# Performance work log

Hardware: AMD Instinct MI355X
Metric: run time of the kernel (lower is better)

## Reference

```python
import jax, jax.numpy as jnp
import numpy as np

N_HEAD, D_MODEL, D_HEAD = 16, 1024, 64
LN_EPS = 1e-5


def setup_inputs() -> dict:
    key = jax.random.key(0)
    ks = jax.random.split(key, 12)
    S, B = 1024, 8
    nd = N_HEAD * D_HEAD
    sc = 0.02
    return {
        "hidden_states": jax.random.normal(ks[0], (S, B, D_MODEL), jnp.float32),
        "rel_pos_emb": jax.random.normal(ks[1], (S, D_MODEL), jnp.float32),
        "encoder_hidden_states": jax.random.normal(ks[2], (S, B, D_MODEL), jnp.float32),
        "W_q": jax.random.normal(ks[3], (D_MODEL, nd), jnp.float32) * sc,
        "W_kv": jax.random.normal(ks[4], (D_MODEL, 2 * nd), jnp.float32) * sc,
        "W_r": jax.random.normal(ks[5], (D_MODEL, nd), jnp.float32) * sc,
        "W_o": jax.random.normal(ks[6], (nd, D_MODEL), jnp.float32) * sc,
        "r_w_bias": jax.random.normal(ks[7], (N_HEAD, D_HEAD), jnp.float32) * sc,
        "r_r_bias": jax.random.normal(ks[8], (N_HEAD, D_HEAD), jnp.float32) * sc,
        "ln_gamma": jnp.ones((D_MODEL,), jnp.float32),
        "ln_beta": jnp.zeros((D_MODEL,), jnp.float32),
    }


def _rel_shift(x):
    # x: (qlen, rlen, bsz, n_head) -- Transformer-XL relative shift trick
    q, r, b, n = x.shape
    zero_pad = jnp.zeros((q, 1, b, n), x.dtype)
    x_padded = jnp.concatenate([zero_pad, x], axis=1).reshape(r + 1, q, b, n)
    return x_padded[1:].reshape(q, r, b, n)


def _layer_norm(x, gamma, beta):
    mu = jnp.mean(x, axis=-1, keepdims=True)
    var = jnp.mean(jnp.square(x - mu), axis=-1, keepdims=True)
    return (x - mu) * jax.lax.rsqrt(var + LN_EPS) * gamma + beta


def reference(hidden_states, rel_pos_emb, encoder_hidden_states,
              W_q, W_kv, W_r, W_o, r_w_bias, r_r_bias, ln_gamma, ln_beta):
    qlen, bsz, _ = hidden_states.shape
    rlen = rel_pos_emb.shape[0]
    # post-lnorm path (pre_lnorm=False), no mems, no mask, eval (dropout off)
    mem_heads = encoder_hidden_states @ W_kv            # (klen, b, 2*n*d)
    w_head_q = hidden_states @ W_q                      # (qlen, b, n*d)
    r_head_k = rel_pos_emb @ W_r                        # (rlen, n*d)
    w_head_k, w_head_v = jnp.split(mem_heads, 2, axis=-1)
    klen = w_head_k.shape[0]

    w_head_q = w_head_q.reshape(qlen, bsz, N_HEAD, D_HEAD)
    w_head_k = w_head_k.reshape(klen, bsz, N_HEAD, D_HEAD)
    w_head_v = w_head_v.reshape(klen, bsz, N_HEAD, D_HEAD)
    r_head_k = r_head_k.reshape(rlen, N_HEAD, D_HEAD)

    scale = 1.0 / (D_HEAD ** 0.5)
    AC = jnp.einsum('ibnd,jbnd->ijbn', w_head_q + r_w_bias, w_head_k)
    BD = jnp.einsum('ibnd,jnd->ijbn', w_head_q + r_r_bias, r_head_k)
    BD = _rel_shift(BD)
    attn_score = (AC + BD) * scale                      # (q, k, b, n)

    attn_prob = jax.nn.softmax(attn_score, axis=1)
    attn_vec = jnp.einsum('ijbn,jbnd->ibnd', attn_prob, w_head_v)
    attn_vec = attn_vec.reshape(qlen, bsz, N_HEAD * D_HEAD)
    attn_out = attn_vec @ W_o
    return _layer_norm(hidden_states + attn_out, ln_gamma, ln_beta)
```

## Files before the change

kernel.cpp:

```cpp
#include <hip/hip_runtime.h>
#include <stdint.h>

constexpr int SEQ = 1024;
constexpr int BSZ = 8;
constexpr int NHEAD = 16;
constexpr int DHEAD = 64;
constexpr int DMODEL = 1024;

using u16 = unsigned short;
using bf16x8 = __attribute__((ext_vector_type(8))) short;
using f32x4 = __attribute__((ext_vector_type(4))) float;

__device__ __forceinline__ float bf2f(u16 u) {
  union { unsigned int i; float f; } c; c.i = ((unsigned int)u) << 16; return c.f;
}
__device__ __forceinline__ unsigned cvtpk(float a, float b) {
  unsigned r; asm("v_cvt_pk_bf16_f32 %0, %1, %2" : "=v"(r) : "v"(a), "v"(b)); return r;
}
__device__ __forceinline__ float exp2v(float x) {
  float r; asm("v_exp_f32 %0, %1" : "=v"(r) : "v"(x)); return r;
}
__device__ __forceinline__ void gload16(const void* g, void* l) {
  __builtin_amdgcn_global_load_lds((const __attribute__((address_space(1))) void*)g,
                                   (__attribute__((address_space(3))) void*)l, 16, 0, 0);
}
__device__ __forceinline__ bf16x8 cvt8(const float* src) {
  f32x4 a = *(const f32x4*)src;
  f32x4 b = *(const f32x4*)(src + 4);
  union { unsigned u[4]; bf16x8 v; } o;
  o.u[0] = cvtpk(a[0], a[1]); o.u[1] = cvtpk(a[2], a[3]);
  o.u[2] = cvtpk(b[0], b[1]); o.u[3] = cvtpk(b[2], b[3]);
  return o.v;
}
__device__ __forceinline__ bf16x8 rd8(const u16* base, int row, int col) {
  return *(const bf16x8*)((const char*)base + (((row * 64 + col) * 2) ^ ((row & 7) << 4)));
}
__device__ __forceinline__ bf16x8 rd8_128(const u16* base, int row, int col) {
  return *(const bf16x8*)((const char*)base + (((row * 128 + col) * 2) ^ ((row & 7) << 4)));
}
__device__ __forceinline__ void wr128(u16* base, int row, int col, u16 v) {
  *(u16*)((char*)base + (((row * 128 + col) * 2) ^ ((row & 7) << 4))) = v;
}

__device__ __forceinline__ void gemm_body_a32(
    const float* __restrict__ A, const u16* __restrict__ BT, u16* __restrict__ C,
    int ldc, int bx, int by, u16* As, u16* Bs) {
  const int t = threadIdx.x;
  const int lane = t & 63;
  const int w = t >> 6, wr = w >> 1, wc = w & 1;
  const int l15 = lane & 15, l4 = lane >> 4;
  const int row0 = by * 128, col0 = bx * 128;
  f32x4 acc[4][4] = {};
  for (int k0 = 0; k0 < 1024; k0 += 64) {
#pragma unroll
    for (int q = 0; q < 4; q++) {
      int u = q * 256 + t;
      int r = u >> 3, c8 = u & 7;
      int sc8 = c8 ^ (r & 7);
      int ub = (q * 256 + (t & ~63)) * 8;
      gload16(BT + (size_t)(col0 + r) * 1024 + k0 + sc8 * 8, Bs + ub);
      const float* src = A + (size_t)(row0 + r) * 1024 + k0 + sc8 * 8;
      *(bf16x8*)(As + (size_t)u * 8) = cvt8(src);
    }
    __syncthreads();
#pragma unroll
    for (int kk = 0; kk < 2; kk++) {
      bf16x8 av[4], bv[4];
#pragma unroll
      for (int f = 0; f < 4; f++) {
        int kb = kk * 32 + l4 * 8;
        av[f] = rd8(As, wr * 64 + f * 16 + l15, kb);
        bv[f] = rd8(Bs, wc * 64 + f * 16 + l15, kb);
      }
#pragma unroll
      for (int fr = 0; fr < 4; fr++)
#pragma unroll
        for (int fc = 0; fc < 4; fc++)
          acc[fr][fc] = __builtin_amdgcn_mfma_f32_16x16x32_bf16(av[fr], bv[fc], acc[fr][fc], 0, 0, 0);
    }
    __syncthreads();
  }
#pragma unroll
  for (int fr = 0; fr < 4; fr++)
#pragma unroll
    for (int fc = 0; fc < 4; fc++) {
      int col = col0 + wc * 64 + fc * 16 + l15;
      int rw0 = row0 + wr * 64 + fr * 16 + l4 * 4;
      unsigned p01 = cvtpk(acc[fr][fc][0], acc[fr][fc][1]);
      unsigned p23 = cvtpk(acc[fr][fc][2], acc[fr][fc][3]);
      C[(size_t)(rw0 + 0) * ldc + col] = (u16)p01;
      C[(size_t)(rw0 + 1) * ldc + col] = (u16)(p01 >> 16);
      C[(size_t)(rw0 + 2) * ldc + col] = (u16)p23;
      C[(size_t)(rw0 + 3) * ldc + col] = (u16)(p23 >> 16);
    }
}

__global__ __launch_bounds__(256, 2) void gemm3(
    const float* __restrict__ hidden, const float* __restrict__ enc,
    const float* __restrict__ relpos,
    const u16* __restrict__ WQT, const u16* __restrict__ WKVT, const u16* __restrict__ WRT,
    u16* __restrict__ Qb, u16* __restrict__ KVb, u16* __restrict__ Rh) {
  __shared__ __align__(16) u16 As[128 * 64];
  __shared__ __align__(16) u16 Bs[128 * 64];
  const int bid = blockIdx.x;
  const float* A; const u16* BT; u16* C; int ldc, bx, by;
  if (bid < 512)       { A = hidden; BT = WQT;  C = Qb;  ldc = 1024; bx = bid & 7;  by = bid >> 3; }
  else if (bid < 1536) { int r = bid - 512;  A = enc;    BT = WKVT; C = KVb; ldc = 2048; bx = r & 15; by = r >> 4; }
  else                 { int r = bid - 1536; A = relpos; BT = WRT;  C = Rh;  ldc = 1024; bx = r & 7;  by = r >> 3; }
  gemm_body_a32(A, BT, C, ldc, bx, by, As, Bs);
}

__global__ __launch_bounds__(256, 2) void gemm_o(
    const u16* __restrict__ Ap, const u16* __restrict__ BT, float* __restrict__ Cp) {
  __shared__ __align__(16) u16 As[128 * 64];
  __shared__ __align__(16) u16 Bs[128 * 64];
  const int t = threadIdx.x;
  const int lane = t & 63;
  const int w = t >> 6, wr = w >> 1, wc = w & 1;
  const int l15 = lane & 15, l4 = lane >> 4;
  const int row0 = blockIdx.y * 128, col0 = blockIdx.x * 128;
  f32x4 acc[4][4] = {};
  for (int k0 = 0; k0 < 1024; k0 += 64) {
#pragma unroll
    for (int q = 0; q < 4; q++) {
      int u = q * 256 + t;
      int r = u >> 3, c8 = u & 7;
      int sc8 = c8 ^ (r & 7);
      int ub = (q * 256 + (t & ~63)) * 8;
      gload16(BT + (size_t)(col0 + r) * 1024 + k0 + sc8 * 8, Bs + ub);
      gload16(Ap + (size_t)(row0 + r) * 1024 + k0 + sc8 * 8, As + ub);
    }
    __syncthreads();
#pragma unroll
    for (int kk = 0; kk < 2; kk++) {
      bf16x8 av[4], bv[4];
#pragma unroll
      for (int f = 0; f < 4; f++) {
        int kb = kk * 32 + l4 * 8;
        av[f] = rd8(As, wr * 64 + f * 16 + l15, kb);
        bv[f] = rd8(Bs, wc * 64 + f * 16 + l15, kb);
      }
#pragma unroll
      for (int fr = 0; fr < 4; fr++)
#pragma unroll
        for (int fc = 0; fc < 4; fc++)
          acc[fr][fc] = __builtin_amdgcn_mfma_f32_16x16x32_bf16(av[fr], bv[fc], acc[fr][fc], 0, 0, 0);
    }
    __syncthreads();
  }
#pragma unroll
  for (int fr = 0; fr < 4; fr++)
#pragma unroll
    for (int fc = 0; fc < 4; fc++) {
      int col = col0 + wc * 64 + fc * 16 + l15;
      int rw0 = row0 + wr * 64 + fr * 16 + l4 * 4;
#pragma unroll
      for (int r = 0; r < 4; r++)
        Cp[(size_t)(rw0 + r) * 1024 + col] = acc[fr][fc][r];
    }
}

__global__ void corr_kernel(const u16* __restrict__ Rh, const float* __restrict__ rwb,
                            const float* __restrict__ rrb, float* __restrict__ corrR) {
  const int m0 = blockIdx.x * 64, n = blockIdx.y;
  const int t = threadIdx.x, r = t >> 2, q = t & 3;
  float p = 0.f;
#pragma unroll
  for (int e = 0; e < 16; e++) {
    int d = q * 16 + e;
    p += (rrb[n * DHEAD + d] - rwb[n * DHEAD + d]) * bf2f(Rh[(size_t)(m0 + r) * DMODEL + n * DHEAD + d]);
  }
  p += __shfl_xor(p, 1, 4);
  p += __shfl_xor(p, 2, 4);
  if (q == 0) corrR[n * SEQ + m0 + r] = p;
}

__global__ __launch_bounds__(256, 3) void flash_fused(
    const u16* __restrict__ Qb, const u16* __restrict__ KVb,
    const u16* __restrict__ VT, const u16* __restrict__ Rh,
    const float* __restrict__ rwb, const float* __restrict__ corrR,
    u16* __restrict__ AV) {
  __shared__ __align__(16) char smem[49408];
  u16* Qs = (u16*)smem;
  u16* Ks = (u16*)(smem + 8320);
  u16* Vs = (u16*)(smem + 16512);
  u16* Rs = (u16*)(smem + 24704);
  u16* Df = (u16*)(smem + 32896);
  const int t = threadIdx.x;
  const int lane = t & 63;
  const int w = t >> 6;
  const int l15 = lane & 15, l4 = lane >> 4;
  const int bid = blockIdx.x;
  const int sw = (bid & 7) * 256 + (bid >> 3);
  const int i0 = (sw & 15) * 64;
  const int z = sw >> 4, b = z >> 4, n = z & 15;
  const float KSC = 0.18033688f;

#pragma unroll
  for (int p = 0; p < 3; p++) {
    int u = p * 256 + t;
    if (u < 520) {
      int r = u >> 3, c8 = u & 7;
      int sc8 = c8 ^ (r & 7);
      int rq = i0 + r; if (rq > SEQ - 1) rq = SEQ - 1;
      bf16x8 qv = *(const bf16x8*)(Qb + ((size_t)rq * BSZ + b) * DMODEL + n * DHEAD + sc8 * 8);
      f32x4 b0 = *(const f32x4*)(rwb + n * DHEAD + sc8 * 8);
      f32x4 b1 = *(const f32x4*)(rwb + n * DHEAD + sc8 * 8 + 4);
      union { unsigned u4[4]; bf16x8 v; } o;
      o.u4[0] = cvtpk(bf2f((u16)qv[0]) + b0[0], bf2f((u16)qv[1]) + b0[1]);
      o.u4[1] = cvtpk(bf2f((u16)qv[2]) + b0[2], bf2f((u16)qv[3]) + b0[3]);
      o.u4[2] = cvtpk(bf2f((u16)qv[4]) + b1[0], bf2f((u16)qv[5]) + b1[1]);
      o.u4[3] = cvtpk(bf2f((u16)qv[6]) + b1[2], bf2f((u16)qv[7]) + b1[3]);
      *(bf16x8*)(Qs + (size_t)u * 8) = o.v;
    }
  }
  const int baseP = (SEQ - 64) - i0;
  const float* corrn = corrR + n * SEQ;
#pragma unroll
  for (int q = 0; q < 2; q++) {
    int u = q * 256 + t;
    int r = u >> 3, c8 = u & 7;
    int sc8 = c8 ^ (r & 7);
    int ub = (q * 256 + (t & ~63)) * 8;
    gload16(Rh + (size_t)(baseP + r) * DMODEL + n * DHEAD + sc8 * 8, Rs + ub);
  }
  float cP[4];
#pragma unroll
  for (int fc = 0; fc < 4; fc++) cP[fc] = corrn[baseP + fc * 16 + l15];
  __syncthreads();
  {
    f32x4 dp[4] = {};
#pragma unroll
    for (int kk = 0; kk < 2; kk++) {
      int kb = kk * 32 + l4 * 8;
      bf16x8 aQ = rd8(Qs, w * 16 + l15, kb);
#pragma unroll
      for (int fc = 0; fc < 4; fc++)
        dp[fc] = __builtin_amdgcn_mfma_f32_16x16x32_bf16(aQ, rd8(Rs, fc * 16 + l15, kb), dp[fc], 0, 0, 0);
    }
#pragma unroll
    for (int r = 0; r < 4; r++) {
      int row = w * 16 + l4 * 4 + r;
      unsigned d01 = cvtpk(dp[0][r] + cP[0], dp[1][r] + cP[1]);
      unsigned d23 = cvtpk(dp[2][r] + cP[2], dp[3][r] + cP[3]);
      wr128(Df, row, 0 * 16 + l15, (u16)d01);
      wr128(Df, row, 1 * 16 + l15, (u16)(d01 >> 16));
      wr128(Df, row, 2 * 16 + l15, (u16)d23);
      wr128(Df, row, 3 * 16 + l15, (u16)(d23 >> 16));
    }
  }
  f32x4 O[4] = {};
  float M[4], Lp[4];
#pragma unroll
  for (int r = 0; r < 4; r++) { M[r] = -1e30f; Lp[r] = 0.f; }
  float spec = 0.f;

  for (int jj = 0; jj < 16; jj++) {
    const int j0 = jj * 64;
    const int dlt = j0 - i0;
    const int base2 = (dlt < 0) ? dlt + SEQ : dlt;
    const int qo2 = (dlt >= 0) ? 1 : 0;
    const int off = (jj & 1) << 6;
    __syncthreads();
#pragma unroll
    for (int q = 0; q < 2; q++) {
      int u = q * 256 + t;
      int r = u >> 3, c8 = u & 7;
      int sc8 = c8 ^ (r & 7);
      int ub = (q * 256 + (t & ~63)) * 8;
      gload16(KVb + ((size_t)(j0 + r) * BSZ + b) * (2 * DMODEL) + n * DHEAD + sc8 * 8, Ks + ub);
      gload16(VT + ((size_t)(b * NHEAD + n) * DHEAD + r) * SEQ + j0 + sc8 * 8, Vs + ub);
      gload16(Rh + (size_t)(base2 + r) * DMODEL + n * DHEAD + sc8 * 8, Rs + ub);
    }
    float cr[4];
#pragma unroll
    for (int fc = 0; fc < 4; fc++) cr[fc] = corrn[base2 + fc * 16 + l15];
    __syncthreads();
    f32x4 sacc[4] = {}, dnew[4] = {};
    __builtin_amdgcn_s_setprio(1);
#pragma unroll
    for (int kk = 0; kk < 2; kk++) {
      int kb = kk * 32 + l4 * 8;
      int qr0 = w * 16 + l15;
      bf16x8 aQ = rd8(Qs, qr0, kb);
      bf16x8 aD = rd8(Qs, qr0 + qo2, kb);
#pragma unroll
      for (int fc = 0; fc < 4; fc++) {
        int br = fc * 16 + l15;
        sacc[fc] = __builtin_amdgcn_mfma_f32_16x16x32_bf16(aQ, rd8(Ks, br, kb), sacc[fc], 0, 0, 0);
        dnew[fc] = __builtin_amdgcn_mfma_f32_16x16x32_bf16(aD, rd8(Rs, br, kb), dnew[fc], 0, 0, 0);
      }
    }
    __builtin_amdgcn_s_setprio(0);
    const int offn = off ^ 64;
#pragma unroll
    for (int r = 0; r < 4; r++) {
      int row = w * 16 + l4 * 4 + r;
      unsigned d01 = cvtpk(dnew[0][r] + cr[0], dnew[1][r] + cr[1]);
      unsigned d23 = cvtpk(dnew[2][r] + cr[2], dnew[3][r] + cr[3]);
      wr128(Df, row, offn + 0 * 16 + l15, (u16)d01);
      wr128(Df, row, offn + 1 * 16 + l15, (u16)(d01 >> 16));
      wr128(Df, row, offn + 2 * 16 + l15, (u16)d23);
      wr128(Df, row, offn + 3 * 16 + l15, (u16)(d23 >> 16));
    }
    float specnext = 0.f;
    if (w == 3)
      specnext = bf2f(*(const u16*)((const char*)Df + ((63 * 256) | ((((off + 63) * 2) ^ 0x70)))));
    const float fix = (dlt == 64) ? 0.f : spec;
#pragma unroll
    for (int r = 0; r < 4; r++) {
      const int lrow = w * 16 + l4 * 4 + r;
      const int rbase = lrow * 256;
      const int swz = (lrow & 7) << 4;
      float v2[4];
      if (dlt < 0) {
        const int K = off + 63 - lrow;
#pragma unroll
        for (int fc = 0; fc < 4; fc++) {
          int col = (fc * 16 + l15 + K) & 127;
          float bd = bf2f(*(const u16*)((const char*)Df + (rbase | ((col * 2) ^ swz))));
          v2[fc] = (sacc[fc][r] + bd) * KSC;
        }
      } else if (dlt == 0) {
#pragma unroll
        for (int fc = 0; fc < 4; fc++) {
          int dj = fc * 16 + l15 - lrow;
          int ul = (dj <= 0) ? dj + 63 : dj + 62;
          int col = (off + ul) & 127;
          float bd = bf2f(*(const u16*)((const char*)Df + (rbase | ((col * 2) ^ swz))));
          if (dj == 1) bd = 0.f;
          v2[fc] = (sacc[fc][r] + bd) * KSC;
        }
      } else {
        const int K = 62 - lrow;
#pragma unroll
        for (int fc = 0; fc < 4; fc++) {
          int ul = fc * 16 + l15 + K;
          int col = (off + ((ul < 0) ? 0 : ul)) & 127;
          float bd = bf2f(*(const u16*)((const char*)Df + (rbase | ((col * 2) ^ swz))));
          if (ul < 0) bd = fix;
          v2[fc] = (sacc[fc][r] + bd) * KSC;
        }
      }
      float tm = fmaxf(fmaxf(v2[0], v2[1]), fmaxf(v2[2], v2[3]));
      unsigned long long bal = __ballot(tm > M[r] + 11.5f);
      if ((bal >> (l4 * 16)) & 0xFFFFull) {
        for (int mk = 1; mk < 16; mk <<= 1) tm = fmaxf(tm, __shfl_xor(tm, mk, 16));
        float alpha = exp2v(M[r] - tm);
        Lp[r] *= alpha;
#pragma unroll
        for (int fd = 0; fd < 4; fd++) O[fd][r] *= alpha;
        M[r] = tm;
      }
      float e0 = exp2v(v2[0] - M[r]), e1 = exp2v(v2[1] - M[r]);
      float e2 = exp2v(v2[2] - M[r]), e3 = exp2v(v2[3] - M[r]);
      Lp[r] += (e0 + e1) + (e2 + e3);
      unsigned p01 = cvtpk(e0, e1), p23 = cvtpk(e2, e3);
      wr128(Df, lrow, off + 0 * 16 + l15, (u16)p01);
      wr128(Df, lrow, off + 1 * 16 + l15, (u16)(p01 >> 16));
      wr128(Df, lrow, off + 2 * 16 + l15, (u16)p23);
      wr128(Df, lrow, off + 3 * 16 + l15, (u16)(p23 >> 16));
    }
    spec = specnext;
    __builtin_amdgcn_s_setprio(1);
#pragma unroll
    for (int kk = 0; kk < 2; kk++) {
      int kb = kk * 32 + l4 * 8;
      bf16x8 a = rd8_128(Df, w * 16 + l15, off + kb);
#pragma unroll
      for (int fd = 0; fd < 4; fd++)
        O[fd] = __builtin_amdgcn_mfma_f32_16x16x32_bf16(a, rd8(Vs, fd * 16 + l15, kb), O[fd], 0, 0, 0);
    }
    __builtin_amdgcn_s_setprio(0);
  }
  float Lf[4];
#pragma unroll
  for (int r = 0; r < 4; r++) {
    float Lt = Lp[r];
    for (int mk = 1; mk < 16; mk <<= 1) Lt += __shfl_xor(Lt, mk, 16);
    Lf[r] = 1.f / Lt;
  }
#pragma unroll
  for (int fd = 0; fd < 4; fd++) {
    int d = fd * 16 + l15;
    int iq0 = i0 + w * 16 + l4 * 4;
    unsigned p01 = cvtpk(O[fd][0] * Lf[0], O[fd][1] * Lf[1]);
    unsigned p23 = cvtpk(O[fd][2] * Lf[2], O[fd][3] * Lf[3]);
    AV[((size_t)(iq0 + 0) * BSZ + b) * DMODEL + n * DHEAD + d] = (u16)p01;
    AV[((size_t)(iq0 + 1) * BSZ + b) * DMODEL + n * DHEAD + d] = (u16)(p01 >> 16);
    AV[((size_t)(iq0 + 2) * BSZ + b) * DMODEL + n * DHEAD + d] = (u16)p23;
    AV[((size_t)(iq0 + 3) * BSZ + b) * DMODEL + n * DHEAD + d] = (u16)(p23 >> 16);
  }
}

__global__ void wtrans4(const float* __restrict__ W_q, const float* __restrict__ W_kv,
                        const float* __restrict__ W_r, const float* __restrict__ W_o,
                        u16* __restrict__ WQT, u16* __restrict__ WKVT,
                        u16* __restrict__ WRT, u16* __restrict__ WOT) {
  __shared__ unsigned int lds[64][65];
  const int bid = blockIdx.x;
  const float* in; u16* out; int C, cx, cy;
  if (bid < 256)      { in = W_q;  out = WQT;  C = 1024; cx = bid & 15;        cy = bid >> 4; }
  else if (bid < 768) { in = W_kv; out = WKVT; C = 2048; cx = (bid - 256) & 31; cy = (bid - 256) >> 5; }
  else if (bid < 1024){ in = W_r;  out = WRT;  C = 1024; cx = (bid - 768) & 15; cy = (bid - 768) >> 4; }
  else                { in = W_o;  out = WOT;  C = 1024; cx = (bid - 1024) & 15; cy = (bid - 1024) >> 4; }
  const int R = 1024;
  const int t = threadIdx.x;
  const int c0 = cx * 64, r0 = cy * 64;
#pragma unroll
  for (int p = 0; p < 2; p++) {
    int u = p * 256 + t;
    int r = u >> 3, c8 = u & 7;
    const float* src = in + (size_t)(r0 + r) * C + c0 + c8 * 8;
    f32x4 v0 = *(const f32x4*)src;
    f32x4 v1 = *(const f32x4*)(src + 4);
    unsigned q0 = cvtpk(v0[0], v0[1]), q1 = cvtpk(v0[2], v0[3]);
    unsigned q2 = cvtpk(v1[0], v1[1]), q3 = cvtpk(v1[2], v1[3]);
    lds[r][c8 * 8 + 0] = (u16)q0; lds[r][c8 * 8 + 1] = (u16)(q0 >> 16);
    lds[r][c8 * 8 + 2] = (u16)q1; lds[r][c8 * 8 + 3] = (u16)(q1 >> 16);
    lds[r][c8 * 8 + 4] = (u16)q2; lds[r][c8 * 8 + 5] = (u16)(q2 >> 16);
    lds[r][c8 * 8 + 6] = (u16)q3; lds[r][c8 * 8 + 7] = (u16)(q3 >> 16);
  }
  __syncthreads();
#pragma unroll
  for (int p = 0; p < 2; p++) {
    int u = p * 256 + t;
    int r = u >> 3, c8 = u & 7;
    bf16x8 v;
#pragma unroll
    for (int e = 0; e < 8; e++) v[e] = (short)lds[c8 * 8 + e][r];
    *(bf16x8*)(out + (size_t)(c0 + r) * R + r0 + c8 * 8) = v;
  }
}

__global__ void vtrans(const u16* __restrict__ KVb, u16* __restrict__ VT) {
  __shared__ unsigned int lds[64][65];
  const int t = threadIdx.x;
  const int s0 = blockIdx.x * 64, n = blockIdx.y, b = blockIdx.z;
#pragma unroll
  for (int p = 0; p < 2; p++) {
    int u = p * 256 + t;
    int r = u >> 3, c8 = u & 7;
    const u16* src = KVb + ((size_t)(s0 + r) * BSZ + b) * (2 * DMODEL) + DMODEL + n * DHEAD + c8 * 8;
    bf16x8 v = *(const bf16x8*)src;
#pragma unroll
    for (int e = 0; e < 8; e++) lds[r][c8 * 8 + e] = (u16)v[e];
  }
  __syncthreads();
#pragma unroll
  for (int p = 0; p < 2; p++) {
    int u = p * 256 + t;
    int r = u >> 3, c8 = u & 7;
    bf16x8 v;
#pragma unroll
    for (int e = 0; e < 8; e++) v[e] = (short)lds[c8 * 8 + e][r];
    *(bf16x8*)(VT + ((size_t)(b * NHEAD + n) * DHEAD + r) * SEQ + s0 + c8 * 8) = v;
  }
}

__global__ void ln_kernel(const float* __restrict__ hidden,
                          const float* __restrict__ gamma, const float* __restrict__ beta,
                          float* __restrict__ out) {
  __shared__ float wsum[4];
  __shared__ float wvar[4];
  const int row = blockIdx.x;
  const int t = threadIdx.x;
  f32x4 hv = *(const f32x4*)(hidden + (size_t)row * DMODEL + t * 4);
  f32x4 ov = *(const f32x4*)(out + (size_t)row * DMODEL + t * 4);
  float xs[4], sum = 0.f;
#pragma unroll
  for (int e = 0; e < 4; e++) { xs[e] = hv[e] + ov[e]; sum += xs[e]; }
  for (int mk = 1; mk < 64; mk <<= 1) sum += __shfl_xor(sum, mk, 64);
  if ((t & 63) == 0) wsum[t >> 6] = sum;
  __syncthreads();
  float mu = (wsum[0] + wsum[1] + wsum[2] + wsum[3]) * (1.f / DMODEL);
  float var = 0.f;
#pragma unroll
  for (int e = 0; e < 4; e++) { float d = xs[e] - mu; var += d * d; }
  for (int mk = 1; mk < 64; mk <<= 1) var += __shfl_xor(var, mk, 64);
  if ((t & 63) == 0) wvar[t >> 6] = var;
  __syncthreads();
  float rstd = rsqrtf((wvar[0] + wvar[1] + wvar[2] + wvar[3]) * (1.f / DMODEL) + 1e-5f);
  f32x4 res;
#pragma unroll
  for (int e = 0; e < 4; e++) {
    int c = t * 4 + e;
    res[e] = (xs[e] - mu) * rstd * gamma[c] + beta[c];
  }
  *(f32x4*)(out + (size_t)row * DMODEL + t * 4) = res;
}

extern "C" void kernel_launch(void* const* d_in, const int* in_sizes, int n_in,
                              void* d_out, int out_size, void* d_ws, size_t ws_size,
                              hipStream_t stream) {
  const float* hidden = (const float*)d_in[0];
  const float* relpos = (const float*)d_in[1];
  const float* enc    = (const float*)d_in[2];
  const float* W_q    = (const float*)d_in[3];
  const float* W_kv   = (const float*)d_in[4];
  const float* W_r    = (const float*)d_in[5];
  const float* W_o    = (const float*)d_in[6];
  const float* rwb    = (const float*)d_in[7];
  const float* rrb    = (const float*)d_in[8];
  const float* gamma  = (const float*)d_in[9];
  const float* beta   = (const float*)d_in[10];
  float* out = (float*)d_out;

  char* ws = (char*)d_ws;
  size_t off = 0;
  auto alloc = [&](size_t bytes) { char* p = ws + off; off += (bytes + 255) & ~(size_t)255; return p; };
  const size_t MB = 1024 * 1024;
  u16* WOT  = (u16*)alloc(2 * MB);
  u16* Qb   = (u16*)alloc(16 * MB);
  u16* KVb  = (u16*)alloc(32 * MB);
  u16* VT   = (u16*)alloc(16 * MB);
  u16* AV   = (u16*)alloc(16 * MB);
  u16* Rh   = (u16*)alloc(2 * MB);
  float* corrR = (float*)alloc(NHEAD * SEQ * 4);
  u16* WQT  = (u16*)alloc(2 * MB);
  u16* WKVT = (u16*)alloc(4 * MB);
  u16* WRT  = (u16*)alloc(2 * MB);
  (void)ws_size; (void)in_sizes; (void)n_in; (void)out_size;

  dim3 blk(256);
  wtrans4<<<dim3(1280), blk, 0, stream>>>(W_q, W_kv, W_r, W_o, WQT, WKVT, WRT, WOT);
  gemm3<<<dim3(1600), blk, 0, stream>>>(hidden, enc, relpos, WQT, WKVT, WRT, Qb, KVb, Rh);
  corr_kernel<<<dim3(16, NHEAD), blk, 0, stream>>>(Rh, rwb, rrb, corrR);
  vtrans<<<dim3(16, NHEAD, BSZ), blk, 0, stream>>>(KVb, VT);

  flash_fused<<<dim3(16 * BSZ * NHEAD), blk, 0, stream>>>(Qb, KVb, VT, Rh, rwb, corrR, AV);

  gemm_o<<<dim3(8, 64), blk, 0, stream>>>(AV, WOT, out);
  ln_kernel<<<dim3(8192), blk, 0, stream>>>(hidden, gamma, beta, out);
}
```

Measured before the change: 297.8 us.

## Pre-convert activations to bf16 in prep and merge corr into vtrans

Adds a pass to the weight-transpose kernel that converts hidden and encoder activations to bf16 in scratch buffers reused from AV and VT. The Q and KV GEMMs can then load their A tiles with direct global-to-LDS async loads instead of converting fp32 per tile. Without this, each fp32 A tile was re-read and re-converted by every column block. It also folds the corr kernel into the V-transpose launch to remove one launch. The cost is an extra full write and read of the bf16 activations and a runtime branch inside the GEMM body.

```diff
diff --git a/kernel.cpp b/kernel.cpp
--- a/kernel.cpp
+++ b/kernel.cpp
@@ -42,9 +42,9 @@
   *(u16*)((char*)base + (((row * 128 + col) * 2) ^ ((row & 7) << 4))) = v;
 }
 
-__device__ __forceinline__ void gemm_body_a32(
-    const float* __restrict__ A, const u16* __restrict__ BT, u16* __restrict__ C,
-    int ldc, int bx, int by, u16* As, u16* Bs) {
+__device__ __forceinline__ void gemm_body(
+    const void* __restrict__ Ap, int a32, const u16* __restrict__ BT,
+    u16* __restrict__ C, int ldc, int bx, int by, u16* As, u16* Bs) {
   const int t = threadIdx.x;
   const int lane = t & 63;
   const int w = t >> 6, wr = w >> 1, wc = w & 1;
@@ -59,8 +59,12 @@
       int sc8 = c8 ^ (r & 7);
       int ub = (q * 256 + (t & ~63)) * 8;
       gload16(BT + (size_t)(col0 + r) * 1024 + k0 + sc8 * 8, Bs + ub);
-      const float* src = A + (size_t)(row0 + r) * 1024 + k0 + sc8 * 8;
-      *(bf16x8*)(As + (size_t)u * 8) = cvt8(src);
+      if (a32) {
+        const float* src = (const float*)Ap + (size_t)(row0 + r) * 1024 + k0 + sc8 * 8;
+        *(bf16x8*)(As + (size_t)u * 8) = cvt8(src);
+      } else {
+        gload16((const u16*)Ap + (size_t)(row0 + r) * 1024 + k0 + sc8 * 8, As + ub);
+      }
     }
     __syncthreads();
 #pragma unroll
@@ -96,18 +100,18 @@
 }
 
 __global__ __launch_bounds__(256, 2) void gemm3(
-    const float* __restrict__ hidden, const float* __restrict__ enc,
+    const u16* __restrict__ hidden_bf, const u16* __restrict__ enc_bf,
     const float* __restrict__ relpos,
     const u16* __restrict__ WQT, const u16* __restrict__ WKVT, const u16* __restrict__ WRT,
     u16* __restrict__ Qb, u16* __restrict__ KVb, u16* __restrict__ Rh) {
   __shared__ __align__(16) u16 As[128 * 64];
   __shared__ __align__(16) u16 Bs[128 * 64];
   const int bid = blockIdx.x;
-  const float* A; const u16* BT; u16* C; int ldc, bx, by;
-  if (bid < 512)       { A = hidden; BT = WQT;  C = Qb;  ldc = 1024; bx = bid & 7;  by = bid >> 3; }
-  else if (bid < 1536) { int r = bid - 512;  A = enc;    BT = WKVT; C = KVb; ldc = 2048; bx = r & 15; by = r >> 4; }
-  else                 { int r = bid - 1536; A = relpos; BT = WRT;  C = Rh;  ldc = 1024; bx = r & 7;  by = r >> 3; }
-  gemm_body_a32(A, BT, C, ldc, bx, by, As, Bs);
+  const void* A; const u16* BT; u16* C; int ldc, bx, by, a32;
+  if (bid < 512)       { A = hidden_bf; BT = WQT;  C = Qb;  ldc = 1024; bx = bid & 7;  by = bid >> 3; a32 = 0; }
+  else if (bid < 1536) { int r = bid - 512;  A = enc_bf; BT = WKVT; C = KVb; ldc = 2048; bx = r & 15; by = r >> 4; a32 = 0; }
+  else                 { int r = bid - 1536; A = relpos; BT = WRT;  C = Rh;  ldc = 1024; bx = r & 7;  by = r >> 3; a32 = 1; }
+  gemm_body(A, a32, BT, C, ldc, bx, by, As, Bs);
 }
 
 __global__ __launch_bounds__(256, 2) void gemm_o(
@@ -158,21 +162,6 @@
       for (int r = 0; r < 4; r++)
         Cp[(size_t)(rw0 + r) * 1024 + col] = acc[fr][fc][r];
     }
-}
-
-__global__ void corr_kernel(const u16* __restrict__ Rh, const float* __restrict__ rwb,
-                            const float* __restrict__ rrb, float* __restrict__ corrR) {
-  const int m0 = blockIdx.x * 64, n = blockIdx.y;
-  const int t = threadIdx.x, r = t >> 2, q = t & 3;
-  float p = 0.f;
-#pragma unroll
-  for (int e = 0; e < 16; e++) {
-    int d = q * 16 + e;
-    p += (rrb[n * DHEAD + d] - rwb[n * DHEAD + d]) * bf2f(Rh[(size_t)(m0 + r) * DMODEL + n * DHEAD + d]);
-  }
-  p += __shfl_xor(p, 1, 4);
-  p += __shfl_xor(p, 2, 4);
-  if (q == 0) corrR[n * SEQ + m0 + r] = p;
 }
 
 __global__ __launch_bounds__(256, 3) void flash_fused(
@@ -393,19 +382,30 @@
   }
 }
 
-__global__ void wtrans4(const float* __restrict__ W_q, const float* __restrict__ W_kv,
-                        const float* __restrict__ W_r, const float* __restrict__ W_o,
-                        u16* __restrict__ WQT, u16* __restrict__ WKVT,
-                        u16* __restrict__ WRT, u16* __restrict__ WOT) {
+__global__ void prep(const float* __restrict__ W_q, const float* __restrict__ W_kv,
+                     const float* __restrict__ W_r, const float* __restrict__ W_o,
+                     u16* __restrict__ WQT, u16* __restrict__ WKVT,
+                     u16* __restrict__ WRT, u16* __restrict__ WOT,
+                     const float* __restrict__ hidden, const float* __restrict__ enc,
+                     u16* __restrict__ hidden_bf, u16* __restrict__ enc_bf) {
+  const int bid = blockIdx.x;
+  const int t = threadIdx.x;
+  if (bid >= 1280) {
+    int r = bid - 1280;
+    const float* src; u16* dst;
+    if (r < 4096) { src = hidden; dst = hidden_bf; }
+    else          { src = enc;    dst = enc_bf;    r -= 4096; }
+    size_t idx = ((size_t)r * 256 + t) * 8;
+    *(bf16x8*)(dst + idx) = cvt8(src + idx);
+    return;
+  }
   __shared__ unsigned int lds[64][65];
-  const int bid = blockIdx.x;
   const float* in; u16* out; int C, cx, cy;
-  if (bid < 256)      { in = W_q;  out = WQT;  C = 1024; cx = bid & 15;        cy = bid >> 4; }
+  if (bid < 256)      { in = W_q;  out = WQT;  C = 1024; cx = bid & 15;         cy = bid >> 4; }
   else if (bid < 768) { in = W_kv; out = WKVT; C = 2048; cx = (bid - 256) & 31; cy = (bid - 256) >> 5; }
   else if (bid < 1024){ in = W_r;  out = WRT;  C = 1024; cx = (bid - 768) & 15; cy = (bid - 768) >> 4; }
   else                { in = W_o;  out = WOT;  C = 1024; cx = (bid - 1024) & 15; cy = (bid - 1024) >> 4; }
   const int R = 1024;
-  const int t = threadIdx.x;
   const int c0 = cx * 64, r0 = cy * 64;
 #pragma unroll
   for (int p = 0; p < 2; p++) {
@@ -433,10 +433,28 @@
   }
 }
 
-__global__ void vtrans(const u16* __restrict__ KVb, u16* __restrict__ VT) {
+__global__ void vtrans_corr(const u16* __restrict__ KVb, u16* __restrict__ VT,
+                            const u16* __restrict__ Rh, const float* __restrict__ rwb,
+                            const float* __restrict__ rrb, float* __restrict__ corrR) {
+  const int bid = blockIdx.x;
+  const int t = threadIdx.x;
+  if (bid >= 2048) {
+    int rr = bid - 2048;
+    const int m0 = (rr & 15) * 64, n = rr >> 4;
+    const int r = t >> 2, q = t & 3;
+    float p = 0.f;
+#pragma unroll
+    for (int e = 0; e < 16; e++) {
+      int d = q * 16 + e;
+      p += (rrb[n * DHEAD + d] - rwb[n * DHEAD + d]) * bf2f(Rh[(size_t)(m0 + r) * DMODEL + n * DHEAD + d]);
+    }
+    p += __shfl_xor(p, 1, 4);
+    p += __shfl_xor(p, 2, 4);
+    if (q == 0) corrR[n * SEQ + m0 + r] = p;
+    return;
+  }
   __shared__ unsigned int lds[64][65];
-  const int t = threadIdx.x;
-  const int s0 = blockIdx.x * 64, n = blockIdx.y, b = blockIdx.z;
+  const int s0 = (bid & 15) * 64, n = (bid >> 4) & 15, b = bid >> 8;
 #pragma unroll
   for (int p = 0; p < 2; p++) {
     int u = p * 256 + t;
@@ -520,13 +538,15 @@
   u16* WQT  = (u16*)alloc(2 * MB);
   u16* WKVT = (u16*)alloc(4 * MB);
   u16* WRT  = (u16*)alloc(2 * MB);
+  u16* hidden_bf = AV;
+  u16* enc_bf    = VT;
   (void)ws_size; (void)in_sizes; (void)n_in; (void)out_size;
 
   dim3 blk(256);
-  wtrans4<<<dim3(1280), blk, 0, stream>>>(W_q, W_kv, W_r, W_o, WQT, WKVT, WRT, WOT);
-  gemm3<<<dim3(1600), blk, 0, stream>>>(hidden, enc, relpos, WQT, WKVT, WRT, Qb, KVb, Rh);
-  corr_kernel<<<dim3(16, NHEAD), blk, 0, stream>>>(Rh, rwb, rrb, corrR);
-  vtrans<<<dim3(16, NHEAD, BSZ), blk, 0, stream>>>(KVb, VT);
+  prep<<<dim3(9472), blk, 0, stream>>>(W_q, W_kv, W_r, W_o, WQT, WKVT, WRT, WOT,
+                                       hidden, enc, hidden_bf, enc_bf);
+  gemm3<<<dim3(1600), blk, 0, stream>>>(hidden_bf, enc_bf, relpos, WQT, WKVT, WRT, Qb, KVb, Rh);
+  vtrans_corr<<<dim3(2304), blk, 0, stream>>>(KVb, VT, Rh, rwb, rrb, corrR);
 
   flash_fused<<<dim3(16 * BSZ * NHEAD), blk, 0, stream>>>(Qb, KVb, VT, Rh, rwb, corrR, AV);
 
```

Measured after the change: 288.5 us. -3.1%, faster.
